# Optimization experiments

Measured on AMD Instinct MI355X. Metric: run time of the kernel, lower is better.

## Reference

```python
import jax, jax.numpy as jnp
import numpy as np
import math

PHI = (1 + math.sqrt(5)) / 2
COMPRESS_EXP = 2.0 / 3.0
ALPHA_D = 0.01


def c_mag(z):
    return jnp.sqrt(z[..., 0] ** 2 + z[..., 1] ** 2 + 1e-08)


def c_phase(z):
    return jnp.arctan2(z[..., 1], z[..., 0] + 1e-10)


def c_mul(a, b):
    real = a[..., 0] * b[..., 0] - a[..., 1] * b[..., 1]
    imag = a[..., 0] * b[..., 1] + a[..., 1] * b[..., 0]
    return jnp.stack([real, imag], axis=-1)


@jax.custom_vjp
def fractal_compress(mag):
    return jnp.clip(mag, 1e-08) ** COMPRESS_EXP


def _fc_fwd(mag):
    ms = jnp.clip(mag, 1e-08)
    c = ms ** COMPRESS_EXP
    return c, c / (ms + 1e-06)


def _fc_bwd(ratio, g):
    return (g * jnp.minimum(ratio, 2.0),)


fractal_compress.defvjp(_fc_fwd, _fc_bwd)


def converge(z):
    mag = c_mag(z)
    phase = c_phase(z)
    cm = fractal_compress(mag)
    return jnp.stack([cm * jnp.cos(phase), cm * jnp.sin(phase)], axis=-1)


def setup_inputs():
    key = jax.random.key(0)
    Bsz, T, D, S = 4, 512, 1024, 16
    dt_rank = D // 16
    ks = jax.random.split(key, 8)
    scale = 1.0 / PHI

    def u(k, shape):
        fan_in = shape[1]
        lim = scale / math.sqrt(fan_in)
        return jax.random.uniform(k, shape, minval=-lim, maxval=lim, dtype=jnp.float32)

    return {
        "x": jax.random.normal(ks[0], (Bsz, T, D), dtype=jnp.float32),
        "W_in": u(ks[1], (2 * D, D)),
        "W_xproj": u(ks[2], (dt_rank + 4 * S, D)),
        "W_dt": u(ks[3], (D, dt_rank)),
        "b_dt": jax.random.uniform(ks[4], (D,), minval=-0.1, maxval=0.1, dtype=jnp.float32),
        "W_out": u(ks[5], (D, D)),
        "b_out": jax.random.uniform(ks[6], (D,), minval=-0.1, maxval=0.1, dtype=jnp.float32),
        "W_res": u(ks[7], (2 * S, D)),
        "A_log": jnp.log(jnp.linspace(1.0, float(S), S)),
    }


def reference(x, W_in, W_xproj, W_dt, b_dt, W_out, b_out, W_res, A_log):
    Bsz, T, D = x.shape
    S = A_log.shape[0]
    dt_rank = W_dt.shape[1]

    xz = x @ W_in.T                      # [B,T,2D]
    x_in, z = xz[..., :D], xz[..., D:]
    x_in = jax.nn.silu(x_in)
    xp = x_in @ W_xproj.T                # [B,T,dt_rank+4S]
    dt = jax.nn.softplus(xp[..., :dt_rank] @ W_dt.T + b_dt)   # [B,T,D]
    bc = xp[..., dt_rank:].reshape(Bsz, T, 2, S, 2)
    B_all, C_all = bc[:, :, 0], bc[:, :, 1]                    # [B,T,S,2]

    A_neg = -jnp.exp(A_log)              # [S]

    # initial deep state d: differentiated phases, tiny magnitude
    phases = jnp.linspace(0.0, 2 * math.pi * (1 - 1.0 / S), S)
    d0 = jnp.stack([0.01 * jnp.cos(phases), 0.01 * jnp.sin(phases)], axis=-1)
    d0 = jnp.broadcast_to(d0, (Bsz, S, 2)).astype(x.dtype)
    h0 = jnp.zeros((Bsz, D, S, 2), dtype=x.dtype)

    def step(carry, xs):
        h_prev, d_prev = carry
        x_t, dt_t, B_t, C_t = xs        # [B,D], [B,D], [B,S,2], [B,S,2]
        x_complex = (x_t @ W_res.T).reshape(Bsz, S, 2)
        d_read = jax.lax.stop_gradient(d_prev)
        T_gate = jnp.cos((c_phase(x_complex) - c_phase(d_read)) / 2) ** 2  # [B,S]
        d_mag = c_mag(d_read)[..., None]
        d_normed = d_read / (d_mag + 1e-08)
        d_scale = jnp.sqrt(jnp.clip(d_mag, 1e-06, 20.0))
        surfaced = d_normed * d_scale * T_gate[..., None]                  # [B,S,2]

        alpha = jnp.exp(dt_t[..., None] * A_neg)                           # [B,D,S]
        x_full = jnp.stack([x_t, jnp.zeros_like(x_t)], axis=-1)            # [B,D,2]
        Bx = c_mul(B_t[:, None, :, :], x_full[:, :, None, :])              # [B,D,S,2]
        Bx = Bx + surfaced[:, None, :, :]
        Bx = Bx * dt_t[:, :, None, None]                                   # gamma scaling

        h_decayed = h_prev * alpha[..., None]
        released = h_prev * (1.0 - alpha)[..., None]
        comp = jnp.clip(converge(released), -10.0, 10.0)
        comp_avg = comp.mean(axis=1)                                       # [B,S,2]
        d_t = jax.lax.stop_gradient(d_prev) + ALPHA_D * comp_avg
        d_mag_new = c_mag(d_t)[..., None]
        d_t = jnp.where(d_mag_new > 20.0, d_t * (20.0 / d_mag_new), d_t)

        h_t = h_decayed + Bx
        Ch = c_mul(C_t[:, None, :, :], h_t)                                # [B,D,S,2]
        y_t = Ch[..., 0].sum(axis=-1)                                      # [B,D]
        return (h_t, d_t), y_t

    xs = (
        jnp.swapaxes(x_in, 0, 1),
        jnp.swapaxes(dt, 0, 1),
        jnp.swapaxes(B_all, 0, 1),
        jnp.swapaxes(C_all, 0, 1),
    )
    (_, _), ys = jax.lax.scan(step, (h0, d0), xs)
    y = jnp.swapaxes(ys, 0, 1)           # [B,T,D]
    y = y * jax.nn.silu(z)
    return y @ W_out.T + b_out
```

## Files before the change

kernel.cpp:

```cpp
#include <hip/hip_runtime.h>
#include <hip/hip_bf16.h>
#include <math.h>


enum { EPI_NONE=0, EPI_SILU=1, EPI_SPBIAS=2, EPI_BIAS=3 };

template<int EPI>
__device__ __forceinline__ float epi_apply(float v, float b) {
  if constexpr (EPI == EPI_SILU)        { return v / (1.0f + expf(-v)); }
  else if constexpr (EPI == EPI_SPBIAS) { float t = v + b; return fmaxf(t, 0.0f) + log1pf(expf(-fabsf(t))); }
  else if constexpr (EPI == EPI_BIAS)   { return v + b; }
  else return v;
}

template<int EPI, bool HAS_A2>
__global__ __launch_bounds__(256) void gemm_wt(
    const float* __restrict__ A, int lda,
    const float* __restrict__ A2, int lda2,
    const float* __restrict__ W, int ldw,
    const float* __restrict__ bias,
    float* __restrict__ C, int ldc,
    int N, int K)
{
  constexpr int BM = 64, BN = 64, BK = 32, PAD = 4;
  __shared__ float As[BK][BM + PAD];
  __shared__ float Ws[BK][BN + PAD];
  const int m0 = blockIdx.x * BM;
  const int n0 = blockIdx.y * BN;
  const int tid = threadIdx.x;
  const int tx = tid & 15;
  const int ty = tid >> 4;
  const int lm = tid & 63;
  const int lk = (tid >> 6) << 3;

  float4 a0, a1, w0, w1;
  {
    const float* p = A + (size_t)(m0 + lm) * lda + lk;
    a0 = ((const float4*)p)[0]; a1 = ((const float4*)p)[1];
    if (HAS_A2) {
      const float* p2 = A2 + (size_t)(m0 + lm) * lda2 + lk;
      const float4 b0 = ((const float4*)p2)[0], b1 = ((const float4*)p2)[1];
      a0.x*=b0.x; a0.y*=b0.y; a0.z*=b0.z; a0.w*=b0.w;
      a1.x*=b1.x; a1.y*=b1.y; a1.z*=b1.z; a1.w*=b1.w;
    }
    const int n = n0 + lm;
    if (n < N) {
      const float* pw = W + (size_t)n * ldw + lk;
      w0 = ((const float4*)pw)[0]; w1 = ((const float4*)pw)[1];
    } else { w0 = make_float4(0.f,0.f,0.f,0.f); w1 = w0; }
  }

  float acc[4][4] = {{0.f,0.f,0.f,0.f},{0.f,0.f,0.f,0.f},{0.f,0.f,0.f,0.f},{0.f,0.f,0.f,0.f}};
  const int NT = K / BK;

  for (int i = 0; i < NT; ++i) {
    __syncthreads();
    As[lk+0][lm]=a0.x; As[lk+1][lm]=a0.y; As[lk+2][lm]=a0.z; As[lk+3][lm]=a0.w;
    As[lk+4][lm]=a1.x; As[lk+5][lm]=a1.y; As[lk+6][lm]=a1.z; As[lk+7][lm]=a1.w;
    Ws[lk+0][lm]=w0.x; Ws[lk+1][lm]=w0.y; Ws[lk+2][lm]=w0.z; Ws[lk+3][lm]=w0.w;
    Ws[lk+4][lm]=w1.x; Ws[lk+5][lm]=w1.y; Ws[lk+6][lm]=w1.z; Ws[lk+7][lm]=w1.w;
    __syncthreads();
    if (i + 1 < NT) {
      const int k0 = (i + 1) * BK;
      const float* p = A + (size_t)(m0 + lm) * lda + k0 + lk;
      a0 = ((const float4*)p)[0]; a1 = ((const float4*)p)[1];
      if (HAS_A2) {
        const float* p2 = A2 + (size_t)(m0 + lm) * lda2 + k0 + lk;
        const float4 b0 = ((const float4*)p2)[0], b1 = ((const float4*)p2)[1];
        a0.x*=b0.x; a0.y*=b0.y; a0.z*=b0.z; a0.w*=b0.w;
        a1.x*=b1.x; a1.y*=b1.y; a1.z*=b1.z; a1.w*=b1.w;
      }
      const int n = n0 + lm;
      if (n < N) {
        const float* pw = W + (size_t)n * ldw + k0 + lk;
        w0 = ((const float4*)pw)[0]; w1 = ((const float4*)pw)[1];
      } else { w0 = make_float4(0.f,0.f,0.f,0.f); w1 = w0; }
    }
#pragma unroll
    for (int kk = 0; kk < BK; ++kk) {
      const float4 a = *(const float4*)&As[kk][ty << 2];
      const float4 w = *(const float4*)&Ws[kk][tx << 2];
      const float ar[4] = {a.x, a.y, a.z, a.w};
      const float wr[4] = {w.x, w.y, w.z, w.w};
#pragma unroll
      for (int ii = 0; ii < 4; ++ii)
#pragma unroll
        for (int j = 0; j < 4; ++j)
          acc[ii][j] = fmaf(ar[ii], wr[j], acc[ii][j]);
    }
  }

  const int ncol = n0 + (tx << 2);
  float bj[4] = {0.f, 0.f, 0.f, 0.f};
  if constexpr (EPI == EPI_SPBIAS || EPI == EPI_BIAS) {
    if (ncol < N) { const float4 bv = *(const float4*)(bias + ncol); bj[0]=bv.x; bj[1]=bv.y; bj[2]=bv.z; bj[3]=bv.w; }
  }
  if (ncol < N) {
#pragma unroll
    for (int i = 0; i < 4; ++i) {
      float vs[4];
#pragma unroll
      for (int j = 0; j < 4; ++j) vs[j] = epi_apply<EPI>(acc[i][j], bj[j]);
      *(float4*)(C + (size_t)(m0 + (ty << 2) + i) * ldc + ncol) = make_float4(vs[0], vs[1], vs[2], vs[3]);
    }
  }
}

__global__ __launch_bounds__(256) void gemm_dualw(
    const float* __restrict__ A, int lda,
    const float* __restrict__ W1,
    const float* __restrict__ W2, int ldw,
    float* __restrict__ C, int ldc,
    int N, int K)
{
  constexpr int BM = 64, BN = 64, BK = 16, PAD = 4;
  __shared__ float As[BK][BM + PAD];
  __shared__ float Ws[BK][BN + PAD];
  const int m0 = blockIdx.x * BM;
  const int n0 = blockIdx.y * BN;
  const int tid = threadIdx.x;
  const int tx = tid & 15;
  const int ty = tid >> 4;
  const int lm = tid >> 2;
  const int lk = (tid & 3) << 2;

  float acc[4][4] = {{0.f,0.f,0.f,0.f},{0.f,0.f,0.f,0.f},{0.f,0.f,0.f,0.f},{0.f,0.f,0.f,0.f}};

  for (int k0 = 0; k0 < K; k0 += BK) {
    float4 av, wv;
    av = *(const float4*)(A + (size_t)(m0 + lm) * lda + k0 + lk);
    {
      const int n = n0 + lm;
      if (n < N) {
        const float* wp = (n < 128) ? (W1 + (size_t)n * ldw + k0 + lk)
                                    : (W2 + (size_t)(n - 128) * ldw + k0 + lk);
        wv = *(const float4*)wp;
      } else wv = make_float4(0.f, 0.f, 0.f, 0.f);
    }
    __syncthreads();
    As[lk+0][lm] = av.x; As[lk+1][lm] = av.y; As[lk+2][lm] = av.z; As[lk+3][lm] = av.w;
    Ws[lk+0][lm] = wv.x; Ws[lk+1][lm] = wv.y; Ws[lk+2][lm] = wv.z; Ws[lk+3][lm] = wv.w;
    __syncthreads();
#pragma unroll
    for (int kk = 0; kk < BK; ++kk) {
      const float4 a = *(const float4*)&As[kk][ty << 2];
      const float4 w = *(const float4*)&Ws[kk][tx << 2];
      const float ar[4] = {a.x, a.y, a.z, a.w};
      const float wr[4] = {w.x, w.y, w.z, w.w};
#pragma unroll
      for (int i = 0; i < 4; ++i)
#pragma unroll
        for (int j = 0; j < 4; ++j)
          acc[i][j] = fmaf(ar[i], wr[j], acc[i][j]);
    }
  }

  const int ncol = n0 + (tx << 2);
  if (ncol < N) {
#pragma unroll
    for (int i = 0; i < 4; ++i)
      *(float4*)(C + (size_t)(m0 + (ty << 2) + i) * ldc + ncol) =
          make_float4(acc[i][0], acc[i][1], acc[i][2], acc[i][3]);
  }
}

template<int EPI>
__global__ __launch_bounds__(256) void gemm_128x64(
    const float* __restrict__ A, int lda,
    const float* __restrict__ W, int ldw,
    float* __restrict__ C, int ldc, int K)
{
  constexpr int BM = 128, BN = 64, BK = 32, PAD = 4;
  __shared__ float As[BK][BM + PAD];
  __shared__ float Ws[BK][BN + PAD];
  const int m0 = blockIdx.x * BM;
  const int n0 = blockIdx.y * BN;
  const int tid = threadIdx.x;
  const int tx = tid & 15;
  const int ty = tid >> 4;
  const int lmA = tid >> 1;
  const int lkA = (tid & 1) << 4;
  const int lmW = tid & 63;
  const int lkW = (tid >> 6) << 3;

  float4 a0, a1, a2, a3, w0, w1;
  {
    const float* pa = A + (size_t)(m0 + lmA) * lda + lkA;
    a0 = ((const float4*)pa)[0]; a1 = ((const float4*)pa)[1];
    a2 = ((const float4*)pa)[2]; a3 = ((const float4*)pa)[3];
    const float* pw = W + (size_t)(n0 + lmW) * ldw + lkW;
    w0 = ((const float4*)pw)[0]; w1 = ((const float4*)pw)[1];
  }

  float acc[8][4];
#pragma unroll
  for (int i = 0; i < 8; ++i)
#pragma unroll
    for (int j = 0; j < 4; ++j) acc[i][j] = 0.f;

  const int NT = K / BK;
  for (int i = 0; i < NT; ++i) {
    __syncthreads();
    As[lkA+ 0][lmA]=a0.x; As[lkA+ 1][lmA]=a0.y; As[lkA+ 2][lmA]=a0.z; As[lkA+ 3][lmA]=a0.w;
    As[lkA+ 4][lmA]=a1.x; As[lkA+ 5][lmA]=a1.y; As[lkA+ 6][lmA]=a1.z; As[lkA+ 7][lmA]=a1.w;
    As[lkA+ 8][lmA]=a2.x; As[lkA+ 9][lmA]=a2.y; As[lkA+10][lmA]=a2.z; As[lkA+11][lmA]=a2.w;
    As[lkA+12][lmA]=a3.x; As[lkA+13][lmA]=a3.y; As[lkA+14][lmA]=a3.z; As[lkA+15][lmA]=a3.w;
    Ws[lkW+0][lmW]=w0.x; Ws[lkW+1][lmW]=w0.y; Ws[lkW+2][lmW]=w0.z; Ws[lkW+3][lmW]=w0.w;
    Ws[lkW+4][lmW]=w1.x; Ws[lkW+5][lmW]=w1.y; Ws[lkW+6][lmW]=w1.z; Ws[lkW+7][lmW]=w1.w;
    __syncthreads();
    if (i + 1 < NT) {
      const int k0 = (i + 1) * BK;
      const float* pa = A + (size_t)(m0 + lmA) * lda + k0 + lkA;
      a0 = ((const float4*)pa)[0]; a1 = ((const float4*)pa)[1];
      a2 = ((const float4*)pa)[2]; a3 = ((const float4*)pa)[3];
      const float* pw = W + (size_t)(n0 + lmW) * ldw + k0 + lkW;
      w0 = ((const float4*)pw)[0]; w1 = ((const float4*)pw)[1];
    }
#pragma unroll
    for (int kk = 0; kk < BK; ++kk) {
      const float4 x0 = *(const float4*)&As[kk][ty << 3];
      const float4 x1 = *(const float4*)&As[kk][(ty << 3) + 4];
      const float4 w  = *(const float4*)&Ws[kk][tx << 2];
      const float ar[8] = {x0.x,x0.y,x0.z,x0.w,x1.x,x1.y,x1.z,x1.w};
      const float wr[4] = {w.x,w.y,w.z,w.w};
#pragma unroll
      for (int ii = 0; ii < 8; ++ii)
#pragma unroll
        for (int j = 0; j < 4; ++j)
          acc[ii][j] = fmaf(ar[ii], wr[j], acc[ii][j]);
    }
  }

  const int ncol = n0 + (tx << 2);
#pragma unroll
  for (int i = 0; i < 8; ++i) {
    float vs[4];
#pragma unroll
    for (int j = 0; j < 4; ++j) vs[j] = epi_apply<EPI>(acc[i][j], 0.f);
    *(float4*)(C + (size_t)(m0 + (ty << 3) + i) * ldc + ncol) = make_float4(vs[0], vs[1], vs[2], vs[3]);
  }
}

__global__ __launch_bounds__(256) void gemm_dt64(
    const float* __restrict__ A, int lda,
    const float* __restrict__ W,
    const float* __restrict__ bias,
    float* __restrict__ C, int ldc)
{
  __shared__ float As[64][68];
  __shared__ float Ws[64][68];
  const int m0 = blockIdx.x * 64;
  const int n0 = blockIdx.y * 64;
  const int tid = threadIdx.x;
  const int lm = tid & 63;
  const int kq = (tid >> 6) << 4;

  {
    const float* pa = A + (size_t)(m0 + lm) * lda + kq;
    const float4 a0 = ((const float4*)pa)[0];
    const float4 a1 = ((const float4*)pa)[1];
    const float4 a2 = ((const float4*)pa)[2];
    const float4 a3 = ((const float4*)pa)[3];
    const float* pw = W + (size_t)(n0 + lm) * 64 + kq;
    const float4 w0 = ((const float4*)pw)[0];
    const float4 w1 = ((const float4*)pw)[1];
    const float4 w2 = ((const float4*)pw)[2];
    const float4 w3 = ((const float4*)pw)[3];
    As[kq+ 0][lm]=a0.x; As[kq+ 1][lm]=a0.y; As[kq+ 2][lm]=a0.z; As[kq+ 3][lm]=a0.w;
    As[kq+ 4][lm]=a1.x; As[kq+ 5][lm]=a1.y; As[kq+ 6][lm]=a1.z; As[kq+ 7][lm]=a1.w;
    As[kq+ 8][lm]=a2.x; As[kq+ 9][lm]=a2.y; As[kq+10][lm]=a2.z; As[kq+11][lm]=a2.w;
    As[kq+12][lm]=a3.x; As[kq+13][lm]=a3.y; As[kq+14][lm]=a3.z; As[kq+15][lm]=a3.w;
    Ws[kq+ 0][lm]=w0.x; Ws[kq+ 1][lm]=w0.y; Ws[kq+ 2][lm]=w0.z; Ws[kq+ 3][lm]=w0.w;
    Ws[kq+ 4][lm]=w1.x; Ws[kq+ 5][lm]=w1.y; Ws[kq+ 6][lm]=w1.z; Ws[kq+ 7][lm]=w1.w;
    Ws[kq+ 8][lm]=w2.x; Ws[kq+ 9][lm]=w2.y; Ws[kq+10][lm]=w2.z; Ws[kq+11][lm]=w2.w;
    Ws[kq+12][lm]=w3.x; Ws[kq+13][lm]=w3.y; Ws[kq+14][lm]=w3.z; Ws[kq+15][lm]=w3.w;
  }
  __syncthreads();

  const int tx = tid & 15;
  const int ty = tid >> 4;
  float acc[4][4] = {{0.f,0.f,0.f,0.f},{0.f,0.f,0.f,0.f},{0.f,0.f,0.f,0.f},{0.f,0.f,0.f,0.f}};
#pragma unroll 16
  for (int kk = 0; kk < 64; ++kk) {
    const float4 a = *(const float4*)&As[kk][ty << 2];
    const float4 w = *(const float4*)&Ws[kk][tx << 2];
    const float ar[4] = {a.x, a.y, a.z, a.w};
    const float wr[4] = {w.x, w.y, w.z, w.w};
#pragma unroll
    for (int i = 0; i < 4; ++i)
#pragma unroll
      for (int j = 0; j < 4; ++j)
        acc[i][j] = fmaf(ar[i], wr[j], acc[i][j]);
  }

  const int ncol = n0 + (tx << 2);
  const float4 bv = *(const float4*)(bias + ncol);
  const float bj[4] = {bv.x, bv.y, bv.z, bv.w};
#pragma unroll
  for (int i = 0; i < 4; ++i) {
    float vs[4];
#pragma unroll
    for (int j = 0; j < 4; ++j) vs[j] = epi_apply<EPI_SPBIAS>(acc[i][j], bj[j]);
    *(float4*)(C + (size_t)(m0 + (ty << 2) + i) * ldc + ncol) = make_float4(vs[0], vs[1], vs[2], vs[3]);
  }
}

__global__ void zero_kernel(float4* __restrict__ p, int n4) {
  const int i = blockIdx.x * blockDim.x + threadIdx.x;
  if (i < n4) p[i] = make_float4(0.f, 0.f, 0.f, 0.f);
}

__global__ __launch_bounds__(256) void reduce_y(const float4* __restrict__ yp, float4* __restrict__ yo, int n4) {
  const int i = blockIdx.x * blockDim.x + threadIdx.x;
  if (i >= n4) return;
  float4 a = yp[i];
#pragma unroll
  for (int s = 1; s < 16; ++s) {
    const float4 v = yp[(size_t)s * 524288 + i];
    a.x += v.x; a.y += v.y; a.z += v.z; a.w += v.w;
  }
  yo[i] = a;
}

template<int CTRL>
__device__ __forceinline__ float dpp_fadd(float x) {
  const int s = __builtin_amdgcn_update_dpp(0, __float_as_int(x), CTRL, 0xF, 0xF, true);
  return x + __int_as_float(s);
}
__device__ __forceinline__ float wave64_sum_l63(float x) {
  x = dpp_fadd<0x111>(x);
  x = dpp_fadd<0x112>(x);
  x = dpp_fadd<0x114>(x);
  x = dpp_fadd<0x118>(x);
  x = dpp_fadd<0x142>(x);
  x = dpp_fadd<0x143>(x);
  return x;
}

__device__ __forceinline__ void comp_block(const float4& dtv, const float na2,
    const float (&h_r)[4], const float (&h_i)[4], float (&al_out)[4],
    float& wr, float& wi)
{
  const float ta[4] = {dtv.x, dtv.y, dtv.z, dtv.w};
  float sr = 0.f, si = 0.f;
#pragma unroll
  for (int e = 0; e < 4; ++e) {
    const float a = exp2f(ta[e] * na2);
    al_out[e] = a;
    const float om    = 1.0f - a;
    const float rel_r = h_r[e] * om, rel_i = h_i[e] * om;
    const float m2 = fmaf(rel_r, rel_r, fmaf(rel_i, rel_i, 1e-8f));
    const float u  = exp2f(log2f(m2) * (-1.0f / 6.0f));
    const float rr = rel_r + 1e-10f;
    float cr = rr * u;    cr = fminf(fmaxf(cr, -10.f), 10.f);
    float ci = rel_i * u; ci = fminf(fmaxf(ci, -10.f), 10.f);
    sr += cr; si += ci;
  }
  wr = wave64_sum_l63(sr);
  wi = wave64_sum_l63(si);
}

template<bool PARTIAL>
__device__ __forceinline__ void step_update(
    float& d_r, float& d_i, const float avg_r, const float avg_i,
    const float2& cx, const float4& xv, const float4& dtv,
    const float2& Bv, const float2& Cv,
    const float (&alv)[4], float (&h_r)[4], float (&h_i)[4],
    float* py)
{
  d_r = fmaf(0.01f, avg_r, d_r);
  d_i = fmaf(0.01f, avg_i, d_i);
  const float dm2c = fmaf(d_r, d_r, fmaf(d_i, d_i, 1e-8f));
  if (dm2c > 400.f) { const float sc = 20.f * __builtin_amdgcn_rsqf(dm2c); d_r *= sc; d_i *= sc; }

  const float xr2 = cx.x + 1e-10f;
  const float irx = __builtin_amdgcn_rsqf(fmaf(xr2, xr2, fmaf(cx.y, cx.y, 1e-38f)));
  const float dr2 = d_r + 1e-10f;
  const float ird = __builtin_amdgcn_rsqf(fmaf(dr2, dr2, fmaf(d_i, d_i, 1e-38f)));
  const float cosdp = fmaf(xr2, dr2, cx.y * d_i) * irx * ird;
  const float Tg  = 0.5f * (1.0f + cosdp);
  const float md2 = fmaf(d_r, d_r, fmaf(d_i, d_i, 1e-8f));
  const float sf  = Tg * exp2f(log2f(md2) * -0.25f);
  const float s_r = d_r * sf, s_i = d_i * sf;

  const float xa[4] = {xv.x, xv.y, xv.z, xv.w};
  const float ta[4] = {dtv.x, dtv.y, dtv.z, dtv.w};
  float yv[4];
#pragma unroll
  for (int e = 0; e < 4; ++e) {
    const float bx_r = fmaf(Bv.x, xa[e], s_r) * ta[e];
    const float bx_i = fmaf(Bv.y, xa[e], s_i) * ta[e];
    h_r[e] = fmaf(h_r[e], alv[e], bx_r);
    h_i[e] = fmaf(h_i[e], alv[e], bx_i);
    yv[e] = fmaf(Cv.x, h_r[e], -(Cv.y * h_i[e]));
  }
  if (PARTIAL) {
    *(float4*)py = make_float4(yv[0], yv[1], yv[2], yv[3]);
  } else {
#pragma unroll
    for (int e = 0; e < 4; ++e) atomicAdd(py + e, yv[e]);
  }
}

template<int RB, int RO, bool PARTIAL>
__device__ __forceinline__ void period_body(
    const float* __restrict__ px, const float* __restrict__ pdt,
    const float* __restrict__ pB, const float* __restrict__ pC,
    const float* __restrict__ pxc, float* __restrict__ py,
    const float na2, const int lane, const int wid,
    float (*red)[4][4],
    float& d_r, float& d_i,
    float (&h_r)[4], float (&h_i)[4], float (&al)[4],
    float4& x0, float4& t0, float2& B0, float2& C0, float2& c0,
    float4& x1, float4& t1, float2& B1, float2& C1, float2& c1,
    const float4& t2)
{
  const float4 qa = *(const float4*)&red[RB][0][0];
  const float4 qb = *(const float4*)&red[RB][1][0];
  const float4 qc = *(const float4*)&red[RB][2][0];
  const float4 qd = *(const float4*)&red[RB][3][0];

  step_update<PARTIAL>(d_r, d_i,
      (qa.x + qb.x + qc.x + qd.x) * (1.0f / 1024.0f),
      (qa.y + qb.y + qc.y + qd.y) * (1.0f / 1024.0f),
      c0, x0, t0, B0, C0, al, h_r, h_i, py + (size_t)RO * 1024);

  x0 = *(const float4*)(px  + (size_t)(RO + 3) * 2048);
  t0 = *(const float4*)(pdt + (size_t)(RO + 3) * 1024);
  B0 = *(const float2*)(pB  + (RO + 3) * 160);
  C0 = *(const float2*)(pC  + (RO + 3) * 160);
  c0 = *(const float2*)(pxc + (RO + 3) * 160);

  float al1[4], w1r, w1i;
  comp_block(t1, na2, h_r, h_i, al1, w1r, w1i);

  step_update<PARTIAL>(d_r, d_i,
      (qa.z + qb.z + qc.z + qd.z) * (1.0f / 1024.0f),
      (qa.w + qb.w + qc.w + qd.w) * (1.0f / 1024.0f),
      c1, x1, t1, B1, C1, al1, h_r, h_i, py + (size_t)(RO + 1) * 1024);

  x1 = *(const float4*)(px  + (size_t)(RO + 4) * 2048);
  t1 = *(const float4*)(pdt + (size_t)(RO + 4) * 1024);
  B1 = *(const float2*)(pB  + (RO + 4) * 160);
  C1 = *(const float2*)(pC  + (RO + 4) * 160);
  c1 = *(const float2*)(pxc + (RO + 4) * 160);

  float w2r, w2i;
  comp_block(t2, na2, h_r, h_i, al, w2r, w2i);

  if (lane == 63) *(float4*)&red[(RB + 1) % 3][wid][0] = make_float4(w1r, w1i, w2r, w2i);

  asm volatile("s_waitcnt lgkmcnt(0)" ::: "memory");
  __builtin_amdgcn_s_barrier();
  asm volatile("" ::: "memory");
}

template<bool PARTIAL>
__global__ __launch_bounds__(256) void scan_kernel(
    const float* __restrict__ xin,
    const float* __restrict__ xpc,
    const float* __restrict__ dtb,
    const float* __restrict__ A_log,
    float* __restrict__ ybase,
    int T)
{
  const int b = blockIdx.x >> 4;
  const int s = blockIdx.x & 15;
  const int d0 = threadIdx.x << 2;
  const int lane = threadIdx.x & 63;
  const int wid = threadIdx.x >> 6;

  __shared__ __align__(16) float red[3][4][4];

  const float a_s = expf(A_log[s]);
  const float na2 = -a_s * 1.4426950408889634f;
  const float phase = (float)(6.283185307179586 * (double)s / 16.0);
  float d_r = 0.01f * cosf(phase);
  float d_i = 0.01f * sinf(phase);
  float h_r[4] = {0.f,0.f,0.f,0.f};
  float h_i[4] = {0.f,0.f,0.f,0.f};
  float al[4];

  const size_t rb = (size_t)b * T;
  const float* px  = xin + rb * 2048 + d0;
  const float* pdt = dtb + rb * 1024 + d0;
  const float* pB  = xpc + rb * 160 + 64 + 2 * s;
  const float* pC  = xpc + rb * 160 + 96 + 2 * s;
  const float* pxc = xpc + rb * 160 + 128 + 2 * s;
  float* py = PARTIAL ? (ybase + (size_t)s * (4 * 512 * 1024) + rb * 1024 + d0)
                      : (ybase + rb * 1024 + d0);

  float4 xA = *(const float4*)px;
  float4 tA = *(const float4*)pdt;
  float2 BA = *(const float2*)pB;
  float2 CA = *(const float2*)pC;
  float2 cA = *(const float2*)pxc;
  float4 xB = *(const float4*)(px + 2048);
  float4 tB = *(const float4*)(pdt + 1024);
  float2 BB = *(const float2*)(pB + 160);
  float2 CB = *(const float2*)(pC + 160);
  float2 cB = *(const float2*)(pxc + 160);
  float4 xC = *(const float4*)(px + 2 * 2048);
  float4 tC = *(const float4*)(pdt + 2 * 1024);
  float2 BC = *(const float2*)(pB + 2 * 160);
  float2 CC = *(const float2*)(pC + 2 * 160);
  float2 cC = *(const float2*)(pxc + 2 * 160);

  {
    float w0r, w0i;
    comp_block(tA, na2, h_r, h_i, al, w0r, w0i);
    if (lane == 63) *(float4*)&red[0][wid][0] = make_float4(0.f, 0.f, w0r, w0i);
  }
  __syncthreads();

  for (int it = 0; it < 85; ++it) {
    period_body<0, 0, PARTIAL>(px, pdt, pB, pC, pxc, py, na2, lane, wid, red,
        d_r, d_i, h_r, h_i, al,
        xA, tA, BA, CA, cA,  xB, tB, BB, CB, cB,  tC);
    period_body<1, 2, PARTIAL>(px, pdt, pB, pC, pxc, py, na2, lane, wid, red,
        d_r, d_i, h_r, h_i, al,
        xC, tC, BC, CC, cC,  xA, tA, BA, CA, cA,  tB);
    period_body<2, 4, PARTIAL>(px, pdt, pB, pC, pxc, py, na2, lane, wid, red,
        d_r, d_i, h_r, h_i, al,
        xB, tB, BB, CB, cB,  xC, tC, BC, CC, cC,  tA);
    px += 6 * 2048; pdt += 6 * 1024; pB += 6 * 160; pC += 6 * 160; pxc += 6 * 160;
    py += 6 * 1024;
  }
  period_body<0, 0, PARTIAL>(px, pdt, pB, pC, pxc, py, na2, lane, wid, red,
      d_r, d_i, h_r, h_i, al,
      xA, tA, BA, CA, cA,  xB, tB, BB, CB, cB,  tC);
}

extern "C" void kernel_launch(void* const* d_in, const int* in_sizes, int n_in,
                              void* d_out, int out_size, void* d_ws, size_t ws_size,
                              hipStream_t stream) {
  const float* x     = (const float*)d_in[0];
  const float* W_in  = (const float*)d_in[1];
  const float* W_xp  = (const float*)d_in[2];
  const float* W_dt  = (const float*)d_in[3];
  const float* b_dt  = (const float*)d_in[4];
  const float* W_out = (const float*)d_in[5];
  const float* b_out = (const float*)d_in[6];
  const float* W_res = (const float*)d_in[7];
  const float* A_log = (const float*)d_in[8];
  float* out = (float*)d_out;

  float* ws     = (float*)d_ws;
  float* siluxz = ws;
  float* xpc    = siluxz + (size_t)2048 * 2048;
  float* dtb    = xpc    + (size_t)2048 * 160;
  float* ybuf   = dtb    + (size_t)2048 * 1024;
  float* ypart  = ybuf   + (size_t)2048 * 1024;

  const size_t need_bytes = ((size_t)8716288 + (size_t)33554432) * 4;
  const bool use_part = ws_size >= need_bytes;

  gemm_128x64<EPI_SILU><<<dim3(16, 32), 256, 0, stream>>>(
      x, 1024, W_in, 1024, siluxz, 2048, 1024);
  gemm_dualw<<<dim3(32, 3), 256, 0, stream>>>(
      siluxz, 2048, W_xp, W_res, 1024, xpc, 160, 160, 1024);
  gemm_dt64<<<dim3(32, 16), 256, 0, stream>>>(
      xpc, 160, W_dt, b_dt, dtb, 1024);

  if (use_part) {
    scan_kernel<true><<<dim3(64), dim3(256), 0, stream>>>(
        siluxz, xpc, dtb, A_log, ypart, 512);
    reduce_y<<<dim3(2048), 256, 0, stream>>>((const float4*)ypart, (float4*)ybuf, 524288);
  } else {
    zero_kernel<<<dim3(2048), 256, 0, stream>>>((float4*)ybuf, (2048 * 1024) / 4);
    scan_kernel<false><<<dim3(64), dim3(256), 0, stream>>>(
        siluxz, xpc, dtb, A_log, ybuf, 512);
  }

  gemm_wt<EPI_BIAS, true><<<dim3(32, 16), 256, 0, stream>>>(
      ybuf, 1024, siluxz + 1024, 2048, W_out, 1024, b_out, out, 1024, 1024, 1024);
}
```

Baseline: 550.9 us.

## Overlap z-half input GEMM with scan kernel and retile small GEMM

The first GEMM now computes only the x half of the input projection (N=1024). The z half (silu of x·W_in[1024:]) moves into extra blocks of the scan kernel, so it runs on otherwise idle CUs while the 64 latency-bound scan blocks execute at raised priority. The xproj GEMM is retiled to 32x32 tiles so more blocks cover the 160-wide output. The risk is that the GEMM blocks compete with the scan blocks for CU resources or memory bandwidth.

```diff
diff --git a/kernel.cpp b/kernel.cpp
--- a/kernel.cpp
+++ b/kernel.cpp
@@ -106,14 +106,13 @@
   }
 }
 
-__global__ __launch_bounds__(256) void gemm_dualw(
+__global__ __launch_bounds__(256) void gemm_dualw32(
     const float* __restrict__ A, int lda,
     const float* __restrict__ W1,
     const float* __restrict__ W2, int ldw,
-    float* __restrict__ C, int ldc,
-    int N, int K)
-{
-  constexpr int BM = 64, BN = 64, BK = 16, PAD = 4;
+    float* __restrict__ C, int ldc, int K)
+{
+  constexpr int BM = 32, BN = 32, BK = 32, PAD = 4;
   __shared__ float As[BK][BM + PAD];
   __shared__ float Ws[BK][BN + PAD];
   const int m0 = blockIdx.x * BM;
@@ -121,124 +120,41 @@
   const int tid = threadIdx.x;
   const int tx = tid & 15;
   const int ty = tid >> 4;
-  const int lm = tid >> 2;
-  const int lk = (tid & 3) << 2;
-
-  float acc[4][4] = {{0.f,0.f,0.f,0.f},{0.f,0.f,0.f,0.f},{0.f,0.f,0.f,0.f},{0.f,0.f,0.f,0.f}};
-
-  for (int k0 = 0; k0 < K; k0 += BK) {
-    float4 av, wv;
-    av = *(const float4*)(A + (size_t)(m0 + lm) * lda + k0 + lk);
-    {
-      const int n = n0 + lm;
-      if (n < N) {
-        const float* wp = (n < 128) ? (W1 + (size_t)n * ldw + k0 + lk)
-                                    : (W2 + (size_t)(n - 128) * ldw + k0 + lk);
-        wv = *(const float4*)wp;
-      } else wv = make_float4(0.f, 0.f, 0.f, 0.f);
-    }
-    __syncthreads();
-    As[lk+0][lm] = av.x; As[lk+1][lm] = av.y; As[lk+2][lm] = av.z; As[lk+3][lm] = av.w;
-    Ws[lk+0][lm] = wv.x; Ws[lk+1][lm] = wv.y; Ws[lk+2][lm] = wv.z; Ws[lk+3][lm] = wv.w;
-    __syncthreads();
-#pragma unroll
-    for (int kk = 0; kk < BK; ++kk) {
-      const float4 a = *(const float4*)&As[kk][ty << 2];
-      const float4 w = *(const float4*)&Ws[kk][tx << 2];
-      const float ar[4] = {a.x, a.y, a.z, a.w};
-      const float wr[4] = {w.x, w.y, w.z, w.w};
-#pragma unroll
-      for (int i = 0; i < 4; ++i)
-#pragma unroll
-        for (int j = 0; j < 4; ++j)
-          acc[i][j] = fmaf(ar[i], wr[j], acc[i][j]);
-    }
-  }
-
-  const int ncol = n0 + (tx << 2);
-  if (ncol < N) {
-#pragma unroll
-    for (int i = 0; i < 4; ++i)
-      *(float4*)(C + (size_t)(m0 + (ty << 2) + i) * ldc + ncol) =
-          make_float4(acc[i][0], acc[i][1], acc[i][2], acc[i][3]);
-  }
-}
-
-template<int EPI>
-__global__ __launch_bounds__(256) void gemm_128x64(
-    const float* __restrict__ A, int lda,
-    const float* __restrict__ W, int ldw,
-    float* __restrict__ C, int ldc, int K)
-{
-  constexpr int BM = 128, BN = 64, BK = 32, PAD = 4;
-  __shared__ float As[BK][BM + PAD];
-  __shared__ float Ws[BK][BN + PAD];
-  const int m0 = blockIdx.x * BM;
-  const int n0 = blockIdx.y * BN;
-  const int tid = threadIdx.x;
-  const int tx = tid & 15;
-  const int ty = tid >> 4;
-  const int lmA = tid >> 1;
-  const int lkA = (tid & 1) << 4;
-  const int lmW = tid & 63;
-  const int lkW = (tid >> 6) << 3;
-
-  float4 a0, a1, a2, a3, w0, w1;
-  {
-    const float* pa = A + (size_t)(m0 + lmA) * lda + lkA;
-    a0 = ((const float4*)pa)[0]; a1 = ((const float4*)pa)[1];
-    a2 = ((const float4*)pa)[2]; a3 = ((const float4*)pa)[3];
-    const float* pw = W + (size_t)(n0 + lmW) * ldw + lkW;
-    w0 = ((const float4*)pw)[0]; w1 = ((const float4*)pw)[1];
-  }
-
-  float acc[8][4];
-#pragma unroll
-  for (int i = 0; i < 8; ++i)
-#pragma unroll
-    for (int j = 0; j < 4; ++j) acc[i][j] = 0.f;
-
+  const int lm = tid & 31;
+  const int lk = (tid >> 5) << 2;
+
+  const int n = n0 + lm;
+  const float* wrow = (n < 128) ? (W1 + (size_t)n * ldw) : (W2 + (size_t)(n - 128) * ldw);
+
+  float4 av = *(const float4*)(A + (size_t)(m0 + lm) * lda + lk);
+  float4 wv = *(const float4*)(wrow + lk);
+
+  float acc[2][2] = {{0.f,0.f},{0.f,0.f}};
   const int NT = K / BK;
   for (int i = 0; i < NT; ++i) {
     __syncthreads();
-    As[lkA+ 0][lmA]=a0.x; As[lkA+ 1][lmA]=a0.y; As[lkA+ 2][lmA]=a0.z; As[lkA+ 3][lmA]=a0.w;
-    As[lkA+ 4][lmA]=a1.x; As[lkA+ 5][lmA]=a1.y; As[lkA+ 6][lmA]=a1.z; As[lkA+ 7][lmA]=a1.w;
-    As[lkA+ 8][lmA]=a2.x; As[lkA+ 9][lmA]=a2.y; As[lkA+10][lmA]=a2.z; As[lkA+11][lmA]=a2.w;
-    As[lkA+12][lmA]=a3.x; As[lkA+13][lmA]=a3.y; As[lkA+14][lmA]=a3.z; As[lkA+15][lmA]=a3.w;
-    Ws[lkW+0][lmW]=w0.x; Ws[lkW+1][lmW]=w0.y; Ws[lkW+2][lmW]=w0.z; Ws[lkW+3][lmW]=w0.w;
-    Ws[lkW+4][lmW]=w1.x; Ws[lkW+5][lmW]=w1.y; Ws[lkW+6][lmW]=w1.z; Ws[lkW+7][lmW]=w1.w;
+    As[lk+0][lm]=av.x; As[lk+1][lm]=av.y; As[lk+2][lm]=av.z; As[lk+3][lm]=av.w;
+    Ws[lk+0][lm]=wv.x; Ws[lk+1][lm]=wv.y; Ws[lk+2][lm]=wv.z; Ws[lk+3][lm]=wv.w;
     __syncthreads();
     if (i + 1 < NT) {
       const int k0 = (i + 1) * BK;
-      const float* pa = A + (size_t)(m0 + lmA) * lda + k0 + lkA;
-      a0 = ((const float4*)pa)[0]; a1 = ((const float4*)pa)[1];
-      a2 = ((const float4*)pa)[2]; a3 = ((const float4*)pa)[3];
-      const float* pw = W + (size_t)(n0 + lmW) * ldw + k0 + lkW;
-      w0 = ((const float4*)pw)[0]; w1 = ((const float4*)pw)[1];
+      av = *(const float4*)(A + (size_t)(m0 + lm) * lda + k0 + lk);
+      wv = *(const float4*)(wrow + k0 + lk);
     }
 #pragma unroll
     for (int kk = 0; kk < BK; ++kk) {
-      const float4 x0 = *(const float4*)&As[kk][ty << 3];
-      const float4 x1 = *(const float4*)&As[kk][(ty << 3) + 4];
-      const float4 w  = *(const float4*)&Ws[kk][tx << 2];
-      const float ar[8] = {x0.x,x0.y,x0.z,x0.w,x1.x,x1.y,x1.z,x1.w};
-      const float wr[4] = {w.x,w.y,w.z,w.w};
-#pragma unroll
-      for (int ii = 0; ii < 8; ++ii)
-#pragma unroll
-        for (int j = 0; j < 4; ++j)
-          acc[ii][j] = fmaf(ar[ii], wr[j], acc[ii][j]);
-    }
-  }
-
-  const int ncol = n0 + (tx << 2);
-#pragma unroll
-  for (int i = 0; i < 8; ++i) {
-    float vs[4];
-#pragma unroll
-    for (int j = 0; j < 4; ++j) vs[j] = epi_apply<EPI>(acc[i][j], 0.f);
-    *(float4*)(C + (size_t)(m0 + (ty << 3) + i) * ldc + ncol) = make_float4(vs[0], vs[1], vs[2], vs[3]);
-  }
+      const float2 a = *(const float2*)&As[kk][ty << 1];
+      const float2 w = *(const float2*)&Ws[kk][tx << 1];
+      acc[0][0] = fmaf(a.x, w.x, acc[0][0]);
+      acc[0][1] = fmaf(a.x, w.y, acc[0][1]);
+      acc[1][0] = fmaf(a.y, w.x, acc[1][0]);
+      acc[1][1] = fmaf(a.y, w.y, acc[1][1]);
+    }
+  }
+  const int ncol = n0 + (tx << 1);
+  float* pc = C + (size_t)(m0 + (ty << 1)) * ldc + ncol;
+  *(float2*)pc         = make_float2(acc[0][0], acc[0][1]);
+  *(float2*)(pc + ldc) = make_float2(acc[1][0], acc[1][1]);
 }
 
 __global__ __launch_bounds__(256) void gemm_dt64(
@@ -456,79 +372,144 @@
 }
 
 template<bool PARTIAL>
-__global__ __launch_bounds__(256) void scan_kernel(
+__global__ __launch_bounds__(256) void scan_g1b(
     const float* __restrict__ xin,
     const float* __restrict__ xpc,
     const float* __restrict__ dtb,
     const float* __restrict__ A_log,
     float* __restrict__ ybase,
-    int T)
-{
-  const int b = blockIdx.x >> 4;
-  const int s = blockIdx.x & 15;
-  const int d0 = threadIdx.x << 2;
-  const int lane = threadIdx.x & 63;
-  const int wid = threadIdx.x >> 6;
-
-  __shared__ __align__(16) float red[3][4][4];
-
-  const float a_s = expf(A_log[s]);
-  const float na2 = -a_s * 1.4426950408889634f;
-  const float phase = (float)(6.283185307179586 * (double)s / 16.0);
-  float d_r = 0.01f * cosf(phase);
-  float d_i = 0.01f * sinf(phase);
-  float h_r[4] = {0.f,0.f,0.f,0.f};
-  float h_i[4] = {0.f,0.f,0.f,0.f};
-  float al[4];
-
-  const size_t rb = (size_t)b * T;
-  const float* px  = xin + rb * 2048 + d0;
-  const float* pdt = dtb + rb * 1024 + d0;
-  const float* pB  = xpc + rb * 160 + 64 + 2 * s;
-  const float* pC  = xpc + rb * 160 + 96 + 2 * s;
-  const float* pxc = xpc + rb * 160 + 128 + 2 * s;
-  float* py = PARTIAL ? (ybase + (size_t)s * (4 * 512 * 1024) + rb * 1024 + d0)
-                      : (ybase + rb * 1024 + d0);
-
-  float4 xA = *(const float4*)px;
-  float4 tA = *(const float4*)pdt;
-  float2 BA = *(const float2*)pB;
-  float2 CA = *(const float2*)pC;
-  float2 cA = *(const float2*)pxc;
-  float4 xB = *(const float4*)(px + 2048);
-  float4 tB = *(const float4*)(pdt + 1024);
-  float2 BB = *(const float2*)(pB + 160);
-  float2 CB = *(const float2*)(pC + 160);
-  float2 cB = *(const float2*)(pxc + 160);
-  float4 xC = *(const float4*)(px + 2 * 2048);
-  float4 tC = *(const float4*)(pdt + 2 * 1024);
-  float2 BC = *(const float2*)(pB + 2 * 160);
-  float2 CC = *(const float2*)(pC + 2 * 160);
-  float2 cC = *(const float2*)(pxc + 2 * 160);
-
-  {
-    float w0r, w0i;
-    comp_block(tA, na2, h_r, h_i, al, w0r, w0i);
-    if (lane == 63) *(float4*)&red[0][wid][0] = make_float4(0.f, 0.f, w0r, w0i);
-  }
-  __syncthreads();
-
-  for (int it = 0; it < 85; ++it) {
+    int T,
+    const float* __restrict__ xg,
+    const float* __restrict__ Wz,
+    float* __restrict__ Cz)
+{
+  if (blockIdx.x < 64) {
+    __builtin_amdgcn_s_setprio(1);
+
+    const int b = blockIdx.x >> 4;
+    const int s = blockIdx.x & 15;
+    const int d0 = threadIdx.x << 2;
+    const int lane = threadIdx.x & 63;
+    const int wid = threadIdx.x >> 6;
+
+    __shared__ __align__(16) float red[3][4][4];
+
+    const float a_s = expf(A_log[s]);
+    const float na2 = -a_s * 1.4426950408889634f;
+    const float phase = (float)(6.283185307179586 * (double)s / 16.0);
+    float d_r = 0.01f * cosf(phase);
+    float d_i = 0.01f * sinf(phase);
+    float h_r[4] = {0.f,0.f,0.f,0.f};
+    float h_i[4] = {0.f,0.f,0.f,0.f};
+    float al[4];
+
+    const size_t rb = (size_t)b * T;
+    const float* px  = xin + rb * 2048 + d0;
+    const float* pdt = dtb + rb * 1024 + d0;
+    const float* pB  = xpc + rb * 160 + 64 + 2 * s;
+    const float* pC  = xpc + rb * 160 + 96 + 2 * s;
+    const float* pxc = xpc + rb * 160 + 128 + 2 * s;
+    float* py = PARTIAL ? (ybase + (size_t)s * (4 * 512 * 1024) + rb * 1024 + d0)
+                        : (ybase + rb * 1024 + d0);
+
+    float4 xA = *(const float4*)px;
+    float4 tA = *(const float4*)pdt;
+    float2 BA = *(const float2*)pB;
+    float2 CA = *(const float2*)pC;
+    float2 cA = *(const float2*)pxc;
+    float4 xB = *(const float4*)(px + 2048);
+    float4 tB = *(const float4*)(pdt + 1024);
+    float2 BB = *(const float2*)(pB + 160);
+    float2 CB = *(const float2*)(pC + 160);
+    float2 cB = *(const float2*)(pxc + 160);
+    float4 xC = *(const float4*)(px + 2 * 2048);
+    float4 tC = *(const float4*)(pdt + 2 * 1024);
+    float2 BC = *(const float2*)(pB + 2 * 160);
+    float2 CC = *(const float2*)(pC + 2 * 160);
+    float2 cC = *(const float2*)(pxc + 2 * 160);
+
+    {
+      float w0r, w0i;
+      comp_block(tA, na2, h_r, h_i, al, w0r, w0i);
+      if (lane == 63) *(float4*)&red[0][wid][0] = make_float4(0.f, 0.f, w0r, w0i);
+    }
+    __syncthreads();
+
+    for (int it = 0; it < 85; ++it) {
+      period_body<0, 0, PARTIAL>(px, pdt, pB, pC, pxc, py, na2, lane, wid, red,
+          d_r, d_i, h_r, h_i, al,
+          xA, tA, BA, CA, cA,  xB, tB, BB, CB, cB,  tC);
+      period_body<1, 2, PARTIAL>(px, pdt, pB, pC, pxc, py, na2, lane, wid, red,
+          d_r, d_i, h_r, h_i, al,
+          xC, tC, BC, CC, cC,  xA, tA, BA, CA, cA,  tB);
+      period_body<2, 4, PARTIAL>(px, pdt, pB, pC, pxc, py, na2, lane, wid, red,
+          d_r, d_i, h_r, h_i, al,
+          xB, tB, BB, CB, cB,  xC, tC, BC, CC, cC,  tA);
+      px += 6 * 2048; pdt += 6 * 1024; pB += 6 * 160; pC += 6 * 160; pxc += 6 * 160;
+      py += 6 * 1024;
+    }
     period_body<0, 0, PARTIAL>(px, pdt, pB, pC, pxc, py, na2, lane, wid, red,
         d_r, d_i, h_r, h_i, al,
         xA, tA, BA, CA, cA,  xB, tB, BB, CB, cB,  tC);
-    period_body<1, 2, PARTIAL>(px, pdt, pB, pC, pxc, py, na2, lane, wid, red,
-        d_r, d_i, h_r, h_i, al,
-        xC, tC, BC, CC, cC,  xA, tA, BA, CA, cA,  tB);
-    period_body<2, 4, PARTIAL>(px, pdt, pB, pC, pxc, py, na2, lane, wid, red,
-        d_r, d_i, h_r, h_i, al,
-        xB, tB, BB, CB, cB,  xC, tC, BC, CC, cC,  tA);
-    px += 6 * 2048; pdt += 6 * 1024; pB += 6 * 160; pC += 6 * 160; pxc += 6 * 160;
-    py += 6 * 1024;
-  }
-  period_body<0, 0, PARTIAL>(px, pdt, pB, pC, pxc, py, na2, lane, wid, red,
-      d_r, d_i, h_r, h_i, al,
-      xA, tA, BA, CA, cA,  xB, tB, BB, CB, cB,  tC);
+    __builtin_amdgcn_s_setprio(0);
+  } else {
+    constexpr int BK = 32, PAD = 4;
+    __shared__ float As[BK][64 + PAD];
+    __shared__ float Ws[BK][64 + PAD];
+    const int b2 = blockIdx.x - 64;
+    const int m0 = (b2 & 31) << 6;
+    const int n0 = (b2 >> 5) << 6;
+    const int tid = threadIdx.x;
+    const int tx = tid & 15;
+    const int ty = tid >> 4;
+    const int lm = tid & 63;
+    const int lk = (tid >> 6) << 3;
+
+    float4 a0, a1, w0, w1;
+    {
+      const float* p = xg + (size_t)(m0 + lm) * 1024 + lk;
+      a0 = ((const float4*)p)[0]; a1 = ((const float4*)p)[1];
+      const float* pw = Wz + (size_t)(n0 + lm) * 1024 + lk;
+      w0 = ((const float4*)pw)[0]; w1 = ((const float4*)pw)[1];
+    }
+    float acc[4][4] = {{0.f,0.f,0.f,0.f},{0.f,0.f,0.f,0.f},{0.f,0.f,0.f,0.f},{0.f,0.f,0.f,0.f}};
+    const int NT = 1024 / BK;
+    for (int i = 0; i < NT; ++i) {
+      __syncthreads();
+      As[lk+0][lm]=a0.x; As[lk+1][lm]=a0.y; As[lk+2][lm]=a0.z; As[lk+3][lm]=a0.w;
+      As[lk+4][lm]=a1.x; As[lk+5][lm]=a1.y; As[lk+6][lm]=a1.z; As[lk+7][lm]=a1.w;
+      Ws[lk+0][lm]=w0.x; Ws[lk+1][lm]=w0.y; Ws[lk+2][lm]=w0.z; Ws[lk+3][lm]=w0.w;
+      Ws[lk+4][lm]=w1.x; Ws[lk+5][lm]=w1.y; Ws[lk+6][lm]=w1.z; Ws[lk+7][lm]=w1.w;
+      __syncthreads();
+      if (i + 1 < NT) {
+        const int k0 = (i + 1) * BK;
+        const float* p = xg + (size_t)(m0 + lm) * 1024 + k0 + lk;
+        a0 = ((const float4*)p)[0]; a1 = ((const float4*)p)[1];
+        const float* pw = Wz + (size_t)(n0 + lm) * 1024 + k0 + lk;
+        w0 = ((const float4*)pw)[0]; w1 = ((const float4*)pw)[1];
+      }
+#pragma unroll
+      for (int kk = 0; kk < BK; ++kk) {
+        const float4 a = *(const float4*)&As[kk][ty << 2];
+        const float4 w = *(const float4*)&Ws[kk][tx << 2];
+        const float ar[4] = {a.x, a.y, a.z, a.w};
+        const float wr[4] = {w.x, w.y, w.z, w.w};
+#pragma unroll
+        for (int ii = 0; ii < 4; ++ii)
+#pragma unroll
+          for (int j = 0; j < 4; ++j)
+            acc[ii][j] = fmaf(ar[ii], wr[j], acc[ii][j]);
+      }
+    }
+    const int ncol = n0 + (tx << 2);
+#pragma unroll
+    for (int i = 0; i < 4; ++i) {
+      float vs[4];
+#pragma unroll
+      for (int j = 0; j < 4; ++j) vs[j] = epi_apply<EPI_SILU>(acc[i][j], 0.f);
+      *(float4*)(Cz + (size_t)(m0 + (ty << 2) + i) * 2048 + ncol) = make_float4(vs[0], vs[1], vs[2], vs[3]);
+    }
+  }
 }
 
 extern "C" void kernel_launch(void* const* d_in, const int* in_sizes, int n_in,
@@ -555,21 +536,23 @@
   const size_t need_bytes = ((size_t)8716288 + (size_t)33554432) * 4;
   const bool use_part = ws_size >= need_bytes;
 
-  gemm_128x64<EPI_SILU><<<dim3(16, 32), 256, 0, stream>>>(
-      x, 1024, W_in, 1024, siluxz, 2048, 1024);
-  gemm_dualw<<<dim3(32, 3), 256, 0, stream>>>(
-      siluxz, 2048, W_xp, W_res, 1024, xpc, 160, 160, 1024);
+  gemm_wt<EPI_SILU, false><<<dim3(32, 16), 256, 0, stream>>>(
+      x, 1024, nullptr, 0, W_in, 1024, nullptr, siluxz, 2048, 1024, 1024);
+  gemm_dualw32<<<dim3(64, 5), 256, 0, stream>>>(
+      siluxz, 2048, W_xp, W_res, 1024, xpc, 160, 1024);
   gemm_dt64<<<dim3(32, 16), 256, 0, stream>>>(
       xpc, 160, W_dt, b_dt, dtb, 1024);
 
   if (use_part) {
-    scan_kernel<true><<<dim3(64), dim3(256), 0, stream>>>(
-        siluxz, xpc, dtb, A_log, ypart, 512);
+    scan_g1b<true><<<dim3(64 + 512), dim3(256), 0, stream>>>(
+        siluxz, xpc, dtb, A_log, ypart, 512,
+        x, W_in + (size_t)1024 * 1024, siluxz + 1024);
     reduce_y<<<dim3(2048), 256, 0, stream>>>((const float4*)ypart, (float4*)ybuf, 524288);
   } else {
     zero_kernel<<<dim3(2048), 256, 0, stream>>>((float4*)ybuf, (2048 * 1024) / 4);
-    scan_kernel<false><<<dim3(64), dim3(256), 0, stream>>>(
-        siluxz, xpc, dtb, A_log, ybuf, 512);
+    scan_g1b<false><<<dim3(64 + 512), dim3(256), 0, stream>>>(
+        siluxz, xpc, dtb, A_log, ybuf, 512,
+        x, W_in + (size_t)1024 * 1024, siluxz + 1024);
   }
 
   gemm_wt<EPI_BIAS, true><<<dim3(32, 16), 256, 0, stream>>>(
```

Measured after the change: 495.1 us. 1.11x faster.
